# Kernel optimization log

Measured on AMD Instinct MI355X. Metric: run time of the kernel, lower is better.

Reference implementation:

```python
import jax, jax.numpy as jnp
import numpy as np

DIM = 1024
HEADS = 16
DIM_HEAD = 64
INNER = HEADS * DIM_HEAD  # 1024
SCALE = 1.0 / DIM_HEAD ** 0.5


def setup_inputs() -> dict:
    key = jax.random.key(0)
    ks = jax.random.split(key, 5)
    x = jax.random.normal(ks[0], (4, 2048, DIM), dtype=jnp.float32)
    # nn.Linear weights stored as [out, in]; we keep [in, out] for x @ W
    Wq = jax.random.normal(ks[1], (DIM, INNER), dtype=jnp.float32) * (1.0 / np.sqrt(DIM))
    Wkv = jax.random.normal(ks[2], (DIM, 2 * INNER), dtype=jnp.float32) * (1.0 / np.sqrt(DIM))
    Wo = jax.random.normal(ks[3], (INNER, DIM), dtype=jnp.float32) * (1.0 / np.sqrt(INNER))
    bo = jax.random.normal(ks[4], (DIM,), dtype=jnp.float32) * 0.01
    return {"x": x, "Wq": Wq, "Wkv": Wkv, "Wo": Wo, "bo": bo}


def reference(x, Wq, Wkv, Wo, bo):
    b, n, _ = x.shape
    q = x @ Wq                      # [b, n, inner]
    kv = x @ Wkv                    # [b, n, 2*inner]
    k, v = jnp.split(kv, 2, axis=2)
    # 'b n (h d) -> b h n d'
    q = q.reshape(b, n, HEADS, DIM_HEAD).transpose(0, 2, 1, 3)
    k = k.reshape(b, n, HEADS, DIM_HEAD).transpose(0, 2, 1, 3)
    v = v.reshape(b, n, HEADS, DIM_HEAD).transpose(0, 2, 1, 3)
    scores = jnp.einsum('bhid,bhjd->bhij', q, k) * SCALE  # [b,h,n,n]
    attn = jax.nn.softmax(scores, axis=-1)
    out = jnp.einsum('bhij,bhjd->bhid', attn, v)          # [b,h,n,d]
    out = out.transpose(0, 2, 1, 3).reshape(b, n, INNER)  # 'b h n d -> b n (h d)'
    return out @ Wo + bo
```

## Files before the change

### kernel.cpp

```cpp
#include <hip/hip_runtime.h>
#include <hip/hip_bf16.h>

typedef unsigned short u16;
typedef unsigned int u32;
typedef __attribute__((ext_vector_type(8))) short s8v;
typedef __attribute__((ext_vector_type(4))) float f4v;
typedef __attribute__((ext_vector_type(4))) unsigned short u16x4;

#define MFMA16(a,b,c) __builtin_amdgcn_mfma_f32_16x16x32_bf16((a),(b),(c),0,0,0)

#define TOKENS 8192
#define SEQ    2048
#define NH     16
#define DH     64
#define DIMK   1024
#define QPRE   0.18033688f

#if defined(__has_builtin)
#if __has_builtin(__builtin_amdgcn_exp2f)
#define EXP2(x) __builtin_amdgcn_exp2f(x)
#else
#define EXP2(x) __expf((x) * 0.69314718f)
#endif
#else
#define EXP2(x) __expf((x) * 0.69314718f)
#endif

__device__ __forceinline__ u16 f2bf(float x){
  union { float f; u32 u; } v; v.f = x;
  u32 r = v.u + 0x7FFFu + ((v.u >> 16) & 1u);
  return (u16)(r >> 16);
}

__device__ __forceinline__ void gld16(const u16* g, u16* s){
  __builtin_amdgcn_global_load_lds(
      (const __attribute__((address_space(1))) unsigned int*)(const void*)g,
      (__attribute__((address_space(3))) unsigned int*)(void*)s,
      16, 0, 0);
}

__global__ __launch_bounds__(256) void k_cast(const float* __restrict__ src,
                                              u16* __restrict__ dst){
  int i = (blockIdx.x * 256 + threadIdx.x) * 4;
  float4 v = *(const float4*)(src + i);
  u16x4 vh;
  float a[4] = {v.x, v.y, v.z, v.w};
#pragma unroll
  for (int j = 0; j < 4; j++) vh[j] = f2bf(a[j]);
  *(u16x4*)(dst + i) = vh;
}

__global__ __launch_bounds__(256) void k_transpose(const float* __restrict__ s0, int c0,
                                                   const float* __restrict__ s1, int c1,
                                                   int K, u16* __restrict__ dh){
  __shared__ float tile[64][65];
  int nb = blockIdx.x * 64, kb = blockIdx.y * 64;
  int tr = threadIdx.x >> 6, tc = threadIdx.x & 63;
#pragma unroll
  for (int i = 0; i < 16; i++){
    int k = kb + tr + i * 4, n = nb + tc;
    float v = (n < c0) ? s0[(size_t)k * c0 + n] : s1[(size_t)k * c1 + (n - c0)];
    tile[tr + i * 4][tc] = v;
  }
  __syncthreads();
#pragma unroll
  for (int i = 0; i < 16; i++){
    int nl = tr + i * 4, kl = tc;
    dh[(size_t)(nb + nl) * K + (kb + kl)] = f2bf(tile[kl][nl]);
  }
}

__global__ __launch_bounds__(256) void k_gemm(
    const u16* __restrict__ A, const u16* __restrict__ B,
    int mode, const float* __restrict__ bias, float* __restrict__ Cf,
    u16* __restrict__ Qh, u16* __restrict__ Kh, u16* __restrict__ Vth)
{
  __shared__ u16 sA[2][128*32], sB[2][128*32];
  const int tid = threadIdx.x, wave = tid >> 6, lane = tid & 63;
  const int lm = lane & 15, quad = lane >> 4;
  const int m0 = blockIdx.y * 128, n0 = blockIdx.x * 128;
  const int cof = (lane & 3) * 8;
  const int rsub = lane >> 2;

  f4v acc[4][4];
#pragma unroll
  for (int i = 0; i < 4; i++)
#pragma unroll
    for (int j = 0; j < 4; j++) acc[i][j] = (f4v){0.f, 0.f, 0.f, 0.f};

  const int wm = (wave >> 1) * 64, wn = (wave & 1) * 64;

  for (int kc = 0; kc < 16; kc++){
    int k = kc * 64;
#pragma unroll
    for (int cc = 0; cc < 2; cc++)
#pragma unroll
      for (int half = 0; half < 2; half++){
        int rb = wave * 32 + half * 16;
        int r = rb + rsub;
        gld16(A + (size_t)(m0 + r) * DIMK + k + cc * 32 + cof, &sA[cc][rb * 32]);
        gld16(B + (size_t)(n0 + r) * DIMK + k + cc * 32 + cof, &sB[cc][rb * 32]);
      }
    __syncthreads();

#pragma unroll
    for (int cc = 0; cc < 2; cc++){
      s8v ah[4], bh[4];
#pragma unroll
      for (int i = 0; i < 4; i++){
        ah[i] = *(const s8v*)&sA[cc][(wm + i * 16 + lm) * 32 + quad * 8];
        bh[i] = *(const s8v*)&sB[cc][(wn + i * 16 + lm) * 32 + quad * 8];
      }
#pragma unroll
      for (int i = 0; i < 4; i++)
#pragma unroll
        for (int j = 0; j < 4; j++)
          acc[i][j] = MFMA16(ah[i], bh[j], acc[i][j]);
    }
    __syncthreads();
  }

  if (mode == 1){
#pragma unroll
    for (int i = 0; i < 4; i++)
#pragma unroll
      for (int j = 0; j < 4; j++){
        int gn = n0 + wn + j * 16 + lm;
        float bv = bias[gn];
#pragma unroll
        for (int r = 0; r < 4; r++){
          int gm = m0 + wm + i * 16 + quad * 4 + r;
          Cf[(size_t)gm * DIMK + gn] = acc[i][j][r] + bv;
        }
      }
  } else {
#pragma unroll
    for (int i = 0; i < 4; i++)
#pragma unroll
      for (int j = 0; j < 4; j++){
        int gn = n0 + wn + j * 16 + lm;
#pragma unroll
        for (int r = 0; r < 4; r++){
          int gm = m0 + wm + i * 16 + quad * 4 + r;
          float v = acc[i][j][r];
          if (gn < 1024){
            Qh[(size_t)gm * DIMK + gn] = f2bf(v * QPRE);
          } else if (gn < 2048){
            Kh[(size_t)gm * DIMK + (gn - 1024)] = f2bf(v);
          } else {
            int df = gn - 2048;
            int hh = df >> 6, dd = df & 63;
            int bb = gm >> 11, ii = gm & 2047;
            int ip = (ii & ~31) | (((ii & 15) << 1) | ((ii >> 4) & 1));
            Vth[(size_t)((bb * NH + hh) * DH + dd) * SEQ + ip] = f2bf(v);
          }
        }
      }
  }
}

__global__ __launch_bounds__(256, 4) void k_attn(
    const u16* __restrict__ Qh, const u16* __restrict__ Kh, const u16* __restrict__ Vth,
    u16* __restrict__ Oh)
{
  __shared__ u16 sK[2*64*32];
  __shared__ u16 sV[2*64*32];
  __shared__ u16 sP[2*128*32];
  u32* sPd = (u32*)sP;

  const int qt = blockIdx.x, h = blockIdx.y, b = blockIdx.z;
  const int tid = threadIdx.x, wave = tid >> 6, lane = tid & 63;
  const int lm = lane & 15, quad = lane >> 4;
  const int tok0 = b * SEQ + qt * 128;
  const int cof = (lane & 3) * 8;
  const int rsub = lane >> 2;

  s8v qf[2][2];
#pragma unroll
  for (int c = 0; c < 2; c++)
#pragma unroll
    for (int ifr = 0; ifr < 2; ifr++){
      size_t ga = (size_t)(tok0 + wave * 32 + ifr * 16 + lm) * DIMK + h * DH + c * 32 + quad * 8;
      qf[c][ifr] = *(const s8v*)(Qh + ga);
    }

  const f4v fz = (f4v){0.f, 0.f, 0.f, 0.f};

  float lpart[2][4];
  f4v oacc[2][4];
#pragma unroll
  for (int ifr = 0; ifr < 2; ifr++){
#pragma unroll
    for (int r = 0; r < 4; r++) lpart[ifr][r] = 0.f;
#pragma unroll
    for (int fd = 0; fd < 4; fd++) oacc[ifr][fd] = (f4v){0.f, 0.f, 0.f, 0.f};
  }

  for (int kt = 0; kt < 32; kt++){
    int j0 = kt * 64;
#pragma unroll
    for (int c = 0; c < 2; c++){
      size_t gk = (size_t)(b * SEQ + j0 + wave * 16 + rsub) * DIMK + h * DH + c * 32 + cof;
      gld16(Kh + gk, &sK[c * 2048 + wave * 512]);
      size_t gv = (size_t)((b * NH + h) * DH + wave * 16 + rsub) * SEQ + j0 + c * 32 + cof;
      gld16(Vth + gv, &sV[c * 2048 + wave * 512]);
    }
    __syncthreads();

    f4v s[2][4];
#pragma unroll
    for (int fn = 0; fn < 4; fn++){
      s8v kh0 = *(const s8v*)&sK[0 * 2048 + (fn * 16 + lm) * 32 + quad * 8];
      s8v kh1 = *(const s8v*)&sK[1 * 2048 + (fn * 16 + lm) * 32 + quad * 8];
#pragma unroll
      for (int ifr = 0; ifr < 2; ifr++){
        s[ifr][fn] = MFMA16(qf[0][ifr], kh0, fz);
        s[ifr][fn] = MFMA16(qf[1][ifr], kh1, s[ifr][fn]);
      }
    }

#pragma unroll
    for (int ifr = 0; ifr < 2; ifr++){
#pragma unroll
      for (int fn = 0; fn < 4; fn++)
#pragma unroll
        for (int r = 0; r < 4; r++)
          s[ifr][fn][r] = EXP2(s[ifr][fn][r]);
      int rowb = wave * 32 + ifr * 16 + quad * 4;
#pragma unroll
      for (int r = 0; r < 4; r++)
#pragma unroll
        for (int jc = 0; jc < 2; jc++){
          union { float f; u32 u; } a0, a1;
          a0.f = s[ifr][jc * 2 + 0][r];
          a1.f = s[ifr][jc * 2 + 1][r];
          lpart[ifr][r] += a0.f + a1.f;
          sPd[jc * 2048 + (rowb + r) * 16 + lm] = __builtin_amdgcn_perm(a1.u, a0.u, 0x07060302);
        }
    }

#pragma unroll
    for (int c = 0; c < 2; c++)
#pragma unroll
      for (int ifr = 0; ifr < 2; ifr++){
        s8v ph = *(const s8v*)&sP[c * 4096 + (wave * 32 + ifr * 16 + lm) * 32 + quad * 8];
#pragma unroll
        for (int fd = 0; fd < 4; fd++){
          s8v vh = *(const s8v*)&sV[c * 2048 + (fd * 16 + lm) * 32 + quad * 8];
          oacc[ifr][fd] = MFMA16(ph, vh, oacc[ifr][fd]);
        }
      }
    __syncthreads();
  }

#pragma unroll
  for (int ifr = 0; ifr < 2; ifr++){
#pragma unroll
    for (int off = 1; off < 16; off <<= 1)
#pragma unroll
      for (int r = 0; r < 4; r++)
        lpart[ifr][r] += __shfl_xor(lpart[ifr][r], off, 64);
    float inv[4];
#pragma unroll
    for (int r = 0; r < 4; r++) inv[r] = 1.f / lpart[ifr][r];
#pragma unroll
    for (int fd = 0; fd < 4; fd++){
      int dcol = h * DH + fd * 16 + lm;
#pragma unroll
      for (int r = 0; r < 4; r++){
        int tok = tok0 + wave * 32 + ifr * 16 + quad * 4 + r;
        Oh[(size_t)tok * DIMK + dcol] = f2bf(oacc[ifr][fd][r] * inv[r]);
      }
    }
  }
}

extern "C" void kernel_launch(void* const* d_in, const int* in_sizes, int n_in,
                              void* d_out, int out_size, void* d_ws, size_t ws_size,
                              hipStream_t stream) {
  const float* x   = (const float*)d_in[0];
  const float* Wq  = (const float*)d_in[1];
  const float* Wkv = (const float*)d_in[2];
  const float* Wo  = (const float*)d_in[3];
  const float* bo  = (const float*)d_in[4];
  float* out = (float*)d_out;

  char* ws = (char*)d_ws;
  size_t off = 0;
  auto alloc = [&](size_t bytes) -> u16* {
    u16* p = (u16*)(ws + off);
    off += (bytes + 255) & ~(size_t)255;
    return p;
  };
  const size_t TK2 = (size_t)TOKENS * DIMK * 2;
  u16* xh  = alloc(TK2);
  u16* Wh  = alloc((size_t)3072 * DIMK * 2);
  u16* WOh = alloc((size_t)1024 * DIMK * 2);
  u16* Qh  = alloc(TK2);
  u16* Kh  = alloc(TK2);
  u16* Vth = alloc(TK2);
  u16* Oh  = alloc(TK2);

  k_cast<<<dim3((TOKENS * DIMK) / 1024), 256, 0, stream>>>(x, xh);
  k_transpose<<<dim3(48, 16), 256, 0, stream>>>(Wq, 1024, Wkv, 2048, DIMK, Wh);
  k_transpose<<<dim3(16, 16), 256, 0, stream>>>(Wo, 1024, Wo, 1024, DIMK, WOh);
  k_gemm<<<dim3(24, 64), 256, 0, stream>>>(xh, Wh, 0, nullptr, nullptr, Qh, Kh, Vth);
  k_attn<<<dim3(16, NH, 4), 256, 0, stream>>>(Qh, Kh, Vth, Oh);
  k_gemm<<<dim3(8, 64), 256, 0, stream>>>(Oh, WOh, 1, bo, out, nullptr, nullptr, nullptr);
}
```

Before: 302.4 us.

## Split QKV GEMM into larger 256x128 tiles with XCD-aware block mapping

The QKV projection moves to its own kernel with 256x128 output tiles: each wave computes 64 rows against all 128 columns, which doubles reuse of the B tile per load. A 1D grid is remapped so that blocks on the same XCD share column tiles, improving L2 locality. The output-projection GEMM becomes a separate, specialized kernel with the mode branch removed. The larger accumulator of 128 floats per lane raises register pressure, and the grid drops to 768 blocks.

```diff
diff --git a/kernel.cpp b/kernel.cpp
--- a/kernel.cpp
+++ b/kernel.cpp
@@ -70,10 +70,92 @@
   }
 }
 
-__global__ __launch_bounds__(256) void k_gemm(
+__global__ __launch_bounds__(256, 2) void k_gemm_qkv(
     const u16* __restrict__ A, const u16* __restrict__ B,
-    int mode, const float* __restrict__ bias, float* __restrict__ Cf,
     u16* __restrict__ Qh, u16* __restrict__ Kh, u16* __restrict__ Vth)
+{
+  __shared__ u16 sA[2][256*32];
+  __shared__ u16 sB[2][128*32];
+  const int tid = threadIdx.x, wave = tid >> 6, lane = tid & 63;
+  const int lm = lane & 15, quad = lane >> 4;
+
+  const int bid = blockIdx.x;
+  const int xcd = bid & 7, slot = bid >> 3;
+  const int xt = xcd * 3 + slot % 3;
+  const int yt = slot / 3;
+  const int m0 = yt * 256, n0 = xt * 128;
+
+  const int cof = (lane & 3) * 8;
+  const int rsub = lane >> 2;
+
+  f4v acc[4][8];
+#pragma unroll
+  for (int i = 0; i < 4; i++)
+#pragma unroll
+    for (int j = 0; j < 8; j++) acc[i][j] = (f4v){0.f, 0.f, 0.f, 0.f};
+
+  for (int kc = 0; kc < 16; kc++){
+    int k = kc * 64;
+#pragma unroll
+    for (int cc = 0; cc < 2; cc++){
+#pragma unroll
+      for (int half = 0; half < 4; half++){
+        int rb = wave * 64 + half * 16;
+        gld16(A + (size_t)(m0 + rb + rsub) * DIMK + k + cc * 32 + cof, &sA[cc][rb * 32]);
+      }
+#pragma unroll
+      for (int half = 0; half < 2; half++){
+        int rb = wave * 32 + half * 16;
+        gld16(B + (size_t)(n0 + rb + rsub) * DIMK + k + cc * 32 + cof, &sB[cc][rb * 32]);
+      }
+    }
+    __syncthreads();
+
+#pragma unroll
+    for (int cc = 0; cc < 2; cc++){
+      s8v ah[4], bh[8];
+#pragma unroll
+      for (int i = 0; i < 4; i++)
+        ah[i] = *(const s8v*)&sA[cc][(wave * 64 + i * 16 + lm) * 32 + quad * 8];
+#pragma unroll
+      for (int j = 0; j < 8; j++)
+        bh[j] = *(const s8v*)&sB[cc][(j * 16 + lm) * 32 + quad * 8];
+#pragma unroll
+      for (int i = 0; i < 4; i++)
+#pragma unroll
+        for (int j = 0; j < 8; j++)
+          acc[i][j] = MFMA16(ah[i], bh[j], acc[i][j]);
+    }
+    __syncthreads();
+  }
+
+#pragma unroll
+  for (int i = 0; i < 4; i++)
+#pragma unroll
+    for (int j = 0; j < 8; j++){
+      int gn = n0 + j * 16 + lm;
+#pragma unroll
+      for (int r = 0; r < 4; r++){
+        int gm = m0 + wave * 64 + i * 16 + quad * 4 + r;
+        float v = acc[i][j][r];
+        if (gn < 1024){
+          Qh[(size_t)gm * DIMK + gn] = f2bf(v * QPRE);
+        } else if (gn < 2048){
+          Kh[(size_t)gm * DIMK + (gn - 1024)] = f2bf(v);
+        } else {
+          int df = gn - 2048;
+          int hh = df >> 6, dd = df & 63;
+          int bb = gm >> 11, ii = gm & 2047;
+          int ip = (ii & ~31) | (((ii & 15) << 1) | ((ii >> 4) & 1));
+          Vth[(size_t)((bb * NH + hh) * DH + dd) * SEQ + ip] = f2bf(v);
+        }
+      }
+    }
+}
+
+__global__ __launch_bounds__(256) void k_gemm_op(
+    const u16* __restrict__ A, const u16* __restrict__ B,
+    const float* __restrict__ bias, float* __restrict__ Cf)
 {
   __shared__ u16 sA[2][128*32], sB[2][128*32];
   const int tid = threadIdx.x, wave = tid >> 6, lane = tid & 63;
@@ -97,9 +179,8 @@
 #pragma unroll
       for (int half = 0; half < 2; half++){
         int rb = wave * 32 + half * 16;
-        int r = rb + rsub;
-        gld16(A + (size_t)(m0 + r) * DIMK + k + cc * 32 + cof, &sA[cc][rb * 32]);
-        gld16(B + (size_t)(n0 + r) * DIMK + k + cc * 32 + cof, &sB[cc][rb * 32]);
+        gld16(A + (size_t)(m0 + rb + rsub) * DIMK + k + cc * 32 + cof, &sA[cc][rb * 32]);
+        gld16(B + (size_t)(n0 + rb + rsub) * DIMK + k + cc * 32 + cof, &sB[cc][rb * 32]);
       }
     __syncthreads();
 
@@ -120,43 +201,18 @@
     __syncthreads();
   }
 
-  if (mode == 1){
-#pragma unroll
-    for (int i = 0; i < 4; i++)
-#pragma unroll
-      for (int j = 0; j < 4; j++){
-        int gn = n0 + wn + j * 16 + lm;
-        float bv = bias[gn];
-#pragma unroll
-        for (int r = 0; r < 4; r++){
-          int gm = m0 + wm + i * 16 + quad * 4 + r;
-          Cf[(size_t)gm * DIMK + gn] = acc[i][j][r] + bv;
-        }
-      }
-  } else {
-#pragma unroll
-    for (int i = 0; i < 4; i++)
-#pragma unroll
-      for (int j = 0; j < 4; j++){
-        int gn = n0 + wn + j * 16 + lm;
-#pragma unroll
-        for (int r = 0; r < 4; r++){
-          int gm = m0 + wm + i * 16 + quad * 4 + r;
-          float v = acc[i][j][r];
-          if (gn < 1024){
-            Qh[(size_t)gm * DIMK + gn] = f2bf(v * QPRE);
-          } else if (gn < 2048){
-            Kh[(size_t)gm * DIMK + (gn - 1024)] = f2bf(v);
-          } else {
-            int df = gn - 2048;
-            int hh = df >> 6, dd = df & 63;
-            int bb = gm >> 11, ii = gm & 2047;
-            int ip = (ii & ~31) | (((ii & 15) << 1) | ((ii >> 4) & 1));
-            Vth[(size_t)((bb * NH + hh) * DH + dd) * SEQ + ip] = f2bf(v);
-          }
-        }
-      }
-  }
+#pragma unroll
+  for (int i = 0; i < 4; i++)
+#pragma unroll
+    for (int j = 0; j < 4; j++){
+      int gn = n0 + wn + j * 16 + lm;
+      float bv = bias[gn];
+#pragma unroll
+      for (int r = 0; r < 4; r++){
+        int gm = m0 + wm + i * 16 + quad * 4 + r;
+        Cf[(size_t)gm * DIMK + gn] = acc[i][j][r] + bv;
+      }
+    }
 }
 
 __global__ __launch_bounds__(256, 4) void k_attn(
@@ -304,7 +360,7 @@
   k_cast<<<dim3((TOKENS * DIMK) / 1024), 256, 0, stream>>>(x, xh);
   k_transpose<<<dim3(48, 16), 256, 0, stream>>>(Wq, 1024, Wkv, 2048, DIMK, Wh);
   k_transpose<<<dim3(16, 16), 256, 0, stream>>>(Wo, 1024, Wo, 1024, DIMK, WOh);
-  k_gemm<<<dim3(24, 64), 256, 0, stream>>>(xh, Wh, 0, nullptr, nullptr, Qh, Kh, Vth);
+  k_gemm_qkv<<<dim3(24 * 32), 256, 0, stream>>>(xh, Wh, Qh, Kh, Vth);
   k_attn<<<dim3(16, NH, 4), 256, 0, stream>>>(Qh, Kh, Vth, Oh);
-  k_gemm<<<dim3(8, 64), 256, 0, stream>>>(Oh, WOh, 1, bo, out, nullptr, nullptr, nullptr);
-}
+  k_gemm_op<<<dim3(8, 64), 256, 0, stream>>>(Oh, WOh, bo, out);
+}
```

After: 319.1 us. 1.06x slower.
